# Kernel tuning notes

Hardware: AMD Instinct MI355X
Metric: run time of the kernel (lower is better)

## Reference

```python
import jax, jax.numpy as jnp
import numpy as np

D_MODEL = 1024
N_HEADS = 16
FF_DIM = 4096
EPS = 1e-05


def setup_inputs() -> dict:
    key = jax.random.key(0)
    ks = jax.random.split(key, 8)
    B, T, E, F = 4, 2048, D_MODEL, FF_DIM
    s = 0.02
    return {
        "encoder_input": jax.random.normal(ks[0], (B, T, E), jnp.float32),
        "source_padding_masks": jax.random.randint(ks[1], (B, T), 0, 2, jnp.int32),
        "Wq": jax.random.normal(ks[2], (E, E), jnp.float32) * s,
        "Wk": jax.random.normal(ks[3], (E, E), jnp.float32) * s,
        "Wv": jax.random.normal(ks[4], (E, E), jnp.float32) * s,
        "Wo": jax.random.normal(ks[5], (E, E), jnp.float32) * s,
        "w1": jax.random.normal(ks[6], (F, E), jnp.float32) * s,
        "b1": jnp.zeros((F,), jnp.float32),
        "w2": jax.random.normal(ks[7], (E, F), jnp.float32) * s,
        "b2": jnp.zeros((E,), jnp.float32),
        "ln_g": jnp.ones((E,), jnp.float32),
        "ln_b": jnp.zeros((E,), jnp.float32),
    }


def _layer_norm(x, g, b):
    # Faithful to the custom LayerNorm: unbiased std (ddof=1), eps added to sd.
    mean = jnp.mean(x, axis=-1, keepdims=True)
    sd = jnp.std(x, axis=-1, keepdims=True, ddof=1)
    return (x - mean) / (sd + EPS) * g + b


def reference(encoder_input, source_padding_masks, Wq, Wk, Wv, Wo, w1, b1, w2, b2, ln_g, ln_b):
    x = encoder_input
    B, T, E = x.shape
    H, hd = N_HEADS, E // N_HEADS

    q = (x @ Wq.T).reshape(B, T, H, hd).transpose(0, 2, 1, 3)  # [B,H,T,hd]
    k = (x @ Wk.T).reshape(B, T, H, hd).transpose(0, 2, 1, 3)
    v = (x @ Wv.T).reshape(B, T, H, hd).transpose(0, 2, 1, 3)

    scores = jnp.einsum("bhqd,bhkd->bhqk", q, k) / jnp.sqrt(jnp.float32(hd))
    key_mask = source_padding_masks[:, None, None, :]  # [B,1,1,T]
    scores = jnp.where(key_mask == 0, -jnp.inf, scores)
    attn = jax.nn.softmax(scores, axis=-1)
    attn = attn * source_padding_masks[:, None, :, None].astype(attn.dtype)  # query mask post-softmax

    ctx = jnp.einsum("bhqk,bhkd->bhqd", attn, v)
    ctx = ctx.transpose(0, 2, 1, 3).reshape(B, T, E)
    att_out = ctx @ Wo.T

    # residual block 1 (dropout is identity in eval)
    h = _layer_norm(att_out + x, ln_g, ln_b)

    ff = jax.nn.relu(h @ w1.T + b1) @ w2.T + b2
    # residual block 2 (same shared LayerNorm params)
    out = _layer_norm(ff + h, ln_g, ln_b)
    return out
```

## Files before the change

kernel.cpp:

```cpp
#include <hip/hip_runtime.h>
#include <hip/hip_bf16.h>


typedef __attribute__((ext_vector_type(8))) short  short8;
typedef __attribute__((ext_vector_type(4))) float  f32x4;
typedef __attribute__((ext_vector_type(4))) int    i32x4;
typedef __attribute__((ext_vector_type(4))) unsigned short u16x4;

__device__ inline float b2f(unsigned short u) {
    unsigned int x = ((unsigned int)u) << 16;
    return __builtin_bit_cast(float, x);
}
__device__ inline unsigned short f2b(float f) {
    return __builtin_bit_cast(unsigned short, __float2bfloat16(f));
}

__device__ inline void llds16(const unsigned short* g, unsigned short* l) {
    __builtin_amdgcn_global_load_lds(
        (const __attribute__((address_space(1))) unsigned int*)g,
        (__attribute__((address_space(3))) unsigned int*)l, 16, 0, 0);
}

__device__ inline int swz(int row, int col8) {
    return (row << 6) + (((col8 ^ (row >> 1)) & 7) << 3);
}

__global__ __launch_bounds__(256)
void cast_f32_bf16(const float* __restrict__ in, unsigned short* __restrict__ out,
                   int n4)
{
    int i = blockIdx.x * 256 + threadIdx.x;
    if (i >= n4) return;
    f32x4 v = *(const f32x4*)(in + (size_t)i * 4);
    u16x4 o;
    for (int j = 0; j < 4; ++j) o[j] = f2b(v[j]);
    *(u16x4*)(out + (size_t)i * 4) = o;
}

__global__ __launch_bounds__(256)
void mask_bf16(const int* __restrict__ m, unsigned short* __restrict__ mb, int n)
{
    int i = blockIdx.x * 256 + threadIdx.x;
    if (i < n) mb[i] = m[i] ? (unsigned short)0x3F80 : (unsigned short)0;
}

template <int BIAS, int RELU, int QKV>
__global__ __launch_bounds__(512, 2)
void gemm256(const unsigned short* __restrict__ A,
             const unsigned short* __restrict__ W,
             const float* __restrict__ bias,
             const int* __restrict__ mask,
             unsigned short* __restrict__ C0,
             unsigned short* __restrict__ C1,
             unsigned short* __restrict__ C2,
             int M, int N, int K)
{
    __shared__ __attribute__((aligned(16))) unsigned short a_s[2][256 * 64];
    __shared__ __attribute__((aligned(16))) unsigned short b_s[2][256 * 64];

    const int tid  = threadIdx.x;
    const int lane = tid & 63;
    const int w    = tid >> 6;
    const int ln   = lane & 15;
    const int quad = lane >> 4;
    const int wm   = w >> 2, wn = w & 3;
    const int bm   = blockIdx.y, bn = blockIdx.x;

    f32x4 acc[8][4] = {};

    auto stage = [&](int buf, int kt) {
#pragma unroll
        for (int i = 0; i < 4; ++i) {
            int e   = i * 512 + tid;
            int row = e >> 3;
            int c8  = (e & 7) ^ ((e >> 4) & 7);
            llds16(A + (size_t)(bm * 256 + row) * K + kt * 64 + c8 * 8,
                   &a_s[buf][e * 8]);
            llds16(W + (size_t)(bn * 256 + row) * K + kt * 64 + c8 * 8,
                   &b_s[buf][e * 8]);
        }
    };

    const int nkt = K >> 6;
    stage(0, 0);
    for (int kt = 0; kt < nkt; ++kt) {
        const int cur = kt & 1;
        asm volatile("s_waitcnt vmcnt(0)" ::: "memory");
        __builtin_amdgcn_s_barrier();
        if (kt + 1 < nkt) stage(cur ^ 1, kt + 1);
#pragma unroll
        for (int ks = 0; ks < 2; ++ks) {
            short8 af[8], bf_[4];
#pragma unroll
            for (int mt = 0; mt < 8; ++mt)
                af[mt] = *(const short8*)&a_s[cur][swz(wm * 128 + mt * 16 + ln, ks * 4 + quad)];
#pragma unroll
            for (int nt = 0; nt < 4; ++nt)
                bf_[nt] = *(const short8*)&b_s[cur][swz(wn * 64 + nt * 16 + ln, ks * 4 + quad)];
            __builtin_amdgcn_s_setprio(1);
#pragma unroll
            for (int mt = 0; mt < 8; ++mt)
#pragma unroll
                for (int nt = 0; nt < 4; ++nt)
                    acc[mt][nt] = __builtin_amdgcn_mfma_f32_16x16x32_bf16(
                        af[mt], bf_[nt], acc[mt][nt], 0, 0, 0);
            __builtin_amdgcn_s_setprio(0);
        }
    }

    const int crow0 = bm * 256 + wm * 128;
    const int ccol0 = bn * 256 + wn * 64;
    if (QKV) {
        const int seg  = bn >> 2;
        const int lc0  = ccol0 & 1023;
        if (seg < 2) {
            unsigned short* C = seg == 0 ? C0 : C1;
#pragma unroll
            for (int nt = 0; nt < 4; ++nt) {
                int col = lc0 + nt * 16 + ln;
#pragma unroll
                for (int mt = 0; mt < 8; ++mt) {
                    int row0 = crow0 + mt * 16 + quad * 4;
#pragma unroll
                    for (int r = 0; r < 4; ++r)
                        C[(size_t)(row0 + r) * 1024 + col] = f2b(acc[mt][nt][r]);
                }
            }
        } else {
            const int T2 = 2048, H2 = 16;
#pragma unroll
            for (int mt = 0; mt < 8; ++mt) {
                int row0 = crow0 + mt * 16 + quad * 4;
                int bb = row0 >> 11, t0 = row0 & 2047;
                i32x4 mi = *(const i32x4*)&mask[bb * 2048 + t0];
#pragma unroll
                for (int nt = 0; nt < 4; ++nt) {
                    int col = lc0 + nt * 16 + ln;
                    int hh2 = col >> 6, d = col & 63;
                    u16x4 o;
#pragma unroll
                    for (int r = 0; r < 4; ++r)
                        o[r] = mi[r] ? f2b(acc[mt][nt][r]) : (unsigned short)0;
                    *(u16x4*)(C2 + ((size_t)((bb * H2 + hh2) * 64 + d)) * T2 + t0) = o;
                }
            }
        }
    } else {
#pragma unroll
        for (int nt = 0; nt < 4; ++nt) {
            int col = ccol0 + nt * 16 + ln;
            float bv = 0.f;
            if (BIAS) bv = bias[col];
#pragma unroll
            for (int mt = 0; mt < 8; ++mt) {
                int row0 = crow0 + mt * 16 + quad * 4;
#pragma unroll
                for (int r = 0; r < 4; ++r) {
                    float v = acc[mt][nt][r] + bv;
                    if (RELU) v = v > 0.f ? v : 0.f;
                    C0[(size_t)(row0 + r) * N + col] = f2b(v);
                }
            }
        }
    }
}

__global__ __launch_bounds__(512, 2)
void flash_attn3(const unsigned short* __restrict__ Q,
                 const unsigned short* __restrict__ K,
                 const unsigned short* __restrict__ Vt,
                 const unsigned short* __restrict__ mb,
                 const int* __restrict__ mask,
                 unsigned short* __restrict__ O,
                 int T, int H, int E)
{
    __shared__ __attribute__((aligned(16))) unsigned short k_s[2][64 * 64];
    __shared__ __attribute__((aligned(16))) unsigned short v_s[2][64 * 64];
    __shared__ __attribute__((aligned(16))) unsigned short p_s[128 * 64];

    const int ord = blockIdx.x;
    const int wg  = (ord & 7) * 128 + (ord >> 3);
    const int qt  = wg & 15;
    const int h   = (wg >> 4) & 15;
    const int b   = wg >> 8;

    const int tid  = threadIdx.x;
    const int w    = tid >> 6;
    const int lane = tid & 63;
    const int ln   = lane & 15;
    const int quad = lane >> 4;
    const int q0   = qt * 128;
    const unsigned short* vt_b = Vt + (size_t)(b * H + h) * 64 * T;

    {
        int e = tid;
        int row = e >> 3;
        int c8  = (e & 7) ^ ((e >> 4) & 7);
        llds16(K + (size_t)(b * T + row) * E + h * 64 + c8 * 8, &k_s[0][e * 8]);
        llds16(vt_b + (size_t)row * T + c8 * 8, &v_s[0][e * 8]);
    }
    for (int i = 0; i < 2; ++i) {
        int e = i * 512 + tid;
        int row = e >> 3;
        int c8  = (e & 7) ^ ((e >> 4) & 7);
        llds16(Q + (size_t)(b * T + q0 + row) * E + h * 64 + c8 * 8, &p_s[e * 8]);
    }
    __syncthreads();
    short8 aq[2];
    aq[0] = *(const short8*)&p_s[w * 1024 + swz(ln, quad)];
    aq[1] = *(const short8*)&p_s[w * 1024 + swz(ln, 4 + quad)];

    f32x4 Oa[4] = {};
    f32x4 lacc = {};
    const float SCL = 0.125f * 1.44269504f;

    const int nkb = T >> 6;
    for (int kb = 0; kb < nkb; ++kb) {
        const int cur = kb & 1;
        if (kb + 1 < nkb) {
            int e = tid;
            int row = e >> 3;
            int c8  = (e & 7) ^ ((e >> 4) & 7);
            llds16(K + (size_t)(b * T + (kb + 1) * 64 + row) * E + h * 64 + c8 * 8,
                   &k_s[cur ^ 1][e * 8]);
            llds16(vt_b + (size_t)row * T + (kb + 1) * 64 + c8 * 8,
                   &v_s[cur ^ 1][e * 8]);
        }
        short8 mf0 = *(const short8*)&mb[b * T + kb * 64 + quad * 8];
        short8 mf1 = *(const short8*)&mb[b * T + kb * 64 + 32 + quad * 8];

        f32x4 S[4] = {};
        for (int ks = 0; ks < 2; ++ks)
            for (int nt = 0; nt < 4; ++nt) {
                short8 bf_ = *(const short8*)&k_s[cur][swz(nt * 16 + ln, ks * 4 + quad)];
                S[nt] = __builtin_amdgcn_mfma_f32_16x16x32_bf16(aq[ks], bf_, S[nt], 0, 0, 0);
            }
        for (int nt = 0; nt < 4; ++nt)
            for (int r = 0; r < 4; ++r) {
                float p = exp2f(S[nt][r] * SCL);
                p_s[w * 1024 + swz(quad * 4 + r, 2 * nt + (ln >> 3)) + (ln & 7)] = f2b(p);
            }
        short8 ap0 = *(const short8*)&p_s[w * 1024 + swz(ln, quad)];
        short8 ap1 = *(const short8*)&p_s[w * 1024 + swz(ln, 4 + quad)];
        lacc = __builtin_amdgcn_mfma_f32_16x16x32_bf16(ap0, mf0, lacc, 0, 0, 0);
        lacc = __builtin_amdgcn_mfma_f32_16x16x32_bf16(ap1, mf1, lacc, 0, 0, 0);
        for (int nt = 0; nt < 4; ++nt) {
            short8 bv0 = *(const short8*)&v_s[cur][swz(nt * 16 + ln, quad)];
            Oa[nt] = __builtin_amdgcn_mfma_f32_16x16x32_bf16(ap0, bv0, Oa[nt], 0, 0, 0);
            short8 bv1 = *(const short8*)&v_s[cur][swz(nt * 16 + ln, 4 + quad)];
            Oa[nt] = __builtin_amdgcn_mfma_f32_16x16x32_bf16(ap1, bv1, Oa[nt], 0, 0, 0);
        }
        __syncthreads();
    }

    for (int r = 0; r < 4; ++r) {
        int qrow = q0 + w * 16 + quad * 4 + r;
        float inv = mask[b * T + qrow] ? 1.f / lacc[r] : 0.f;
        for (int nt = 0; nt < 4; ++nt)
            O[(size_t)(b * T + qrow) * E + h * 64 + nt * 16 + ln] = f2b(Oa[nt][r] * inv);
    }
}

template <int R_F32, int O_F32>
__global__ __launch_bounds__(256, 4)
void ln_residual(const unsigned short* __restrict__ A,
                 const void* __restrict__ R,
                 const float* __restrict__ G,
                 const float* __restrict__ Bt,
                 void* __restrict__ Y, int E)
{
    const int row = blockIdx.x;
    const int tid = threadIdx.x;
    size_t base = (size_t)row * E + tid * 4;
    u16x4 a4 = *(const u16x4*)(A + base);
    float rv[4];
    if (R_F32) {
        f32x4 r4 = *(const f32x4*)((const float*)R + base);
        for (int j = 0; j < 4; ++j) rv[j] = r4[j];
    } else {
        u16x4 r4 = *(const u16x4*)((const unsigned short*)R + base);
        for (int j = 0; j < 4; ++j) rv[j] = b2f(r4[j]);
    }
    float v[4]; float s = 0.f, sq = 0.f;
    for (int j = 0; j < 4; ++j) {
        v[j] = b2f(a4[j]) + rv[j];
        s += v[j]; sq += v[j] * v[j];
    }
    for (int o = 32; o; o >>= 1) {
        s  += __shfl_xor(s, o, 64);
        sq += __shfl_xor(sq, o, 64);
    }
    __shared__ float red[8];
    int w = tid >> 6, lane = tid & 63;
    if (lane == 0) { red[w] = s; red[4 + w] = sq; }
    __syncthreads();
    s  = red[0] + red[1] + red[2] + red[3];
    sq = red[4] + red[5] + red[6] + red[7];
    float mean = s / E;
    float var  = (sq - s * mean) / (E - 1);
    var = fmaxf(var, 0.f);
    float inv = 1.f / (sqrtf(var) + 1e-5f);
    f32x4 g4 = *(const f32x4*)(G + tid * 4);
    f32x4 b4 = *(const f32x4*)(Bt + tid * 4);
    if (O_F32) {
        f32x4 o4;
        for (int j = 0; j < 4; ++j)
            o4[j] = (v[j] - mean) * inv * g4[j] + b4[j];
        *(f32x4*)((float*)Y + base) = o4;
    } else {
        u16x4 o4;
        for (int j = 0; j < 4; ++j)
            o4[j] = f2b((v[j] - mean) * inv * g4[j] + b4[j]);
        *(u16x4*)((unsigned short*)Y + base) = o4;
    }
}

extern "C" void kernel_launch(void* const* d_in, const int* in_sizes, int n_in,
                              void* d_out, int out_size, void* d_ws, size_t ws_size,
                              hipStream_t stream)
{
    const int B = 4, T = 2048, E = 1024, F = 4096, H = 16;
    const int M = B * T;

    const float* x  = (const float*)d_in[0];
    const int* mask = (const int*)d_in[1];
    const float* Wq = (const float*)d_in[2];
    const float* Wk = (const float*)d_in[3];
    const float* Wv = (const float*)d_in[4];
    const float* Wo = (const float*)d_in[5];
    const float* w1 = (const float*)d_in[6];
    const float* b1 = (const float*)d_in[7];
    const float* w2 = (const float*)d_in[8];
    const float* b2 = (const float*)d_in[9];
    const float* lg = (const float*)d_in[10];
    const float* lb = (const float*)d_in[11];
    float* out = (float*)d_out;

    char* ws = (char*)d_ws;
    const size_t MB = 1024 * 1024;
    unsigned short* xb  = (unsigned short*)(ws);
    unsigned short* q   = (unsigned short*)(ws + 16 * MB);
    unsigned short* kk  = (unsigned short*)(ws + 32 * MB);
    unsigned short* vt  = (unsigned short*)(ws + 48 * MB);
    unsigned short* ctx = (unsigned short*)(ws + 64 * MB);
    unsigned short* hh  = (unsigned short*)(ws + 80 * MB);
    unsigned short* mbf = hh;
    unsigned short* ff1 = (unsigned short*)(ws);
    unsigned short* ff2 = ctx;
    unsigned short* att = q;
    unsigned short* Wqb = (unsigned short*)(ws + 96 * MB);
    unsigned short* Wkb = (unsigned short*)(ws + 98 * MB);
    unsigned short* Wvb = (unsigned short*)(ws + 100 * MB);
    unsigned short* Wob = (unsigned short*)(ws + 102 * MB);
    unsigned short* w1b = (unsigned short*)(ws + 104 * MB);
    unsigned short* w2b = (unsigned short*)(ws + 112 * MB);

    dim3 blk(256);
    cast_f32_bf16<<<dim3(M * E / 4 / 256), blk, 0, stream>>>(x,  xb,  M * E / 4);
    cast_f32_bf16<<<dim3(E * E / 4 / 256), blk, 0, stream>>>(Wq, Wqb, E * E / 4);
    cast_f32_bf16<<<dim3(E * E / 4 / 256), blk, 0, stream>>>(Wk, Wkb, E * E / 4);
    cast_f32_bf16<<<dim3(E * E / 4 / 256), blk, 0, stream>>>(Wv, Wvb, E * E / 4);
    cast_f32_bf16<<<dim3(E * E / 4 / 256), blk, 0, stream>>>(Wo, Wob, E * E / 4);
    cast_f32_bf16<<<dim3(F * E / 4 / 256), blk, 0, stream>>>(w1, w1b, F * E / 4);
    cast_f32_bf16<<<dim3(F * E / 4 / 256), blk, 0, stream>>>(w2, w2b, F * E / 4);
    mask_bf16<<<dim3(M / 256), blk, 0, stream>>>(mask, mbf, M);

    dim3 g512(512);
    gemm256<0, 0, 1><<<dim3(3072 / 256, M / 256), g512, 0, stream>>>(
        xb, Wqb, nullptr, mask, q, kk, vt, M, 3072, E);
    flash_attn3<<<dim3((T / 128) * H * B), g512, 0, stream>>>(q, kk, vt, mbf, mask, ctx, T, H, E);
    gemm256<0, 0, 0><<<dim3(E / 256, M / 256), g512, 0, stream>>>(
        ctx, Wob, nullptr, nullptr, att, nullptr, nullptr, M, E, E);
    ln_residual<1, 0><<<dim3(M), blk, 0, stream>>>(att, x, lg, lb, hh, E);
    gemm256<1, 1, 0><<<dim3(F / 256, M / 256), g512, 0, stream>>>(
        hh, w1b, b1, nullptr, ff1, nullptr, nullptr, M, F, E);
    gemm256<1, 0, 0><<<dim3(E / 256, M / 256), g512, 0, stream>>>(
        ff1, w2b, b2, nullptr, ff2, nullptr, nullptr, M, E, F);
    ln_residual<0, 1><<<dim3(M), blk, 0, stream>>>(ff2, hh, lg, lb, out, E);
}
```

Baseline: 614.3 us.

## Shrink GEMM tiles to 128x128 with deeper prefetch and merge cast launches

The GEMM tile drops from 256x256 with 512 threads to 128x128 with 256 threads. The K-loop now issues loads two tiles ahead and uses a partial vmcnt wait instead of draining all loads each iteration. The seven separate f32-to-bf16 cast launches become one launch that maps block ranges to tensors. The smaller tiles mean more blocks, which fills the CUs better (for example the M=8192, N=1024 GEMMs go from 128 to 512 blocks), at the cost of lower operand reuse per block and an extra barrier each iteration.

```diff
diff --git a/kernel.cpp b/kernel.cpp
--- a/kernel.cpp
+++ b/kernel.cpp
@@ -25,16 +25,23 @@
     return (row << 6) + (((col8 ^ (row >> 1)) & 7) << 3);
 }
 
+struct CastArgs {
+    const float* src[7];
+    unsigned short* dst[7];
+    int blkcum[8];
+};
+
 __global__ __launch_bounds__(256)
-void cast_f32_bf16(const float* __restrict__ in, unsigned short* __restrict__ out,
-                   int n4)
-{
-    int i = blockIdx.x * 256 + threadIdx.x;
-    if (i >= n4) return;
-    f32x4 v = *(const f32x4*)(in + (size_t)i * 4);
+void cast_all(CastArgs a)
+{
+    int blk = blockIdx.x;
+    int s = 0;
+    while (blk >= a.blkcum[s + 1]) ++s;
+    int i = (blk - a.blkcum[s]) * 256 + threadIdx.x;
+    f32x4 v = *(const f32x4*)(a.src[s] + (size_t)i * 4);
     u16x4 o;
     for (int j = 0; j < 4; ++j) o[j] = f2b(v[j]);
-    *(u16x4*)(out + (size_t)i * 4) = o;
+    *(u16x4*)(a.dst[s] + (size_t)i * 4) = o;
 }
 
 __global__ __launch_bounds__(256)
@@ -45,8 +52,8 @@
 }
 
 template <int BIAS, int RELU, int QKV>
-__global__ __launch_bounds__(512, 2)
-void gemm256(const unsigned short* __restrict__ A,
+__global__ __launch_bounds__(256, 2)
+void gemm_db(const unsigned short* __restrict__ A,
              const unsigned short* __restrict__ W,
              const float* __restrict__ bias,
              const int* __restrict__ mask,
@@ -55,72 +62,73 @@
              unsigned short* __restrict__ C2,
              int M, int N, int K)
 {
-    __shared__ __attribute__((aligned(16))) unsigned short a_s[2][256 * 64];
-    __shared__ __attribute__((aligned(16))) unsigned short b_s[2][256 * 64];
+    __shared__ __attribute__((aligned(16))) unsigned short a_s[2][128 * 64];
+    __shared__ __attribute__((aligned(16))) unsigned short b_s[2][128 * 64];
 
     const int tid  = threadIdx.x;
     const int lane = tid & 63;
     const int w    = tid >> 6;
     const int ln   = lane & 15;
     const int quad = lane >> 4;
-    const int wm   = w >> 2, wn = w & 3;
+    const int wm   = w >> 1, wn = w & 1;
     const int bm   = blockIdx.y, bn = blockIdx.x;
 
-    f32x4 acc[8][4] = {};
+    f32x4 acc[4][4] = {};
+
+    const unsigned short* Abase = A + (size_t)(bm * 128) * K;
+    const unsigned short* Wbase = W + (size_t)(bn * 128) * K;
 
     auto stage = [&](int buf, int kt) {
 #pragma unroll
         for (int i = 0; i < 4; ++i) {
-            int e   = i * 512 + tid;
+            int e   = i * 256 + tid;
             int row = e >> 3;
             int c8  = (e & 7) ^ ((e >> 4) & 7);
-            llds16(A + (size_t)(bm * 256 + row) * K + kt * 64 + c8 * 8,
-                   &a_s[buf][e * 8]);
-            llds16(W + (size_t)(bn * 256 + row) * K + kt * 64 + c8 * 8,
-                   &b_s[buf][e * 8]);
+            llds16(Abase + (size_t)row * K + kt * 64 + c8 * 8, &a_s[buf][e * 8]);
+            llds16(Wbase + (size_t)row * K + kt * 64 + c8 * 8, &b_s[buf][e * 8]);
         }
     };
 
     const int nkt = K >> 6;
     stage(0, 0);
+    stage(1, 1);
+    int cur = 0;
     for (int kt = 0; kt < nkt; ++kt) {
-        const int cur = kt & 1;
-        asm volatile("s_waitcnt vmcnt(0)" ::: "memory");
-        __builtin_amdgcn_s_barrier();
-        if (kt + 1 < nkt) stage(cur ^ 1, kt + 1);
+        if (kt + 1 < nkt) asm volatile("s_waitcnt vmcnt(8)" ::: "memory");
+        else              asm volatile("s_waitcnt vmcnt(0)" ::: "memory");
+        asm volatile("s_barrier" ::: "memory");
 #pragma unroll
         for (int ks = 0; ks < 2; ++ks) {
-            short8 af[8], bf_[4];
-#pragma unroll
-            for (int mt = 0; mt < 8; ++mt)
-                af[mt] = *(const short8*)&a_s[cur][swz(wm * 128 + mt * 16 + ln, ks * 4 + quad)];
+            short8 af[4], bf_[4];
+#pragma unroll
+            for (int mt = 0; mt < 4; ++mt)
+                af[mt] = *(const short8*)&a_s[cur][swz(wm * 64 + mt * 16 + ln, ks * 4 + quad)];
 #pragma unroll
             for (int nt = 0; nt < 4; ++nt)
                 bf_[nt] = *(const short8*)&b_s[cur][swz(wn * 64 + nt * 16 + ln, ks * 4 + quad)];
-            __builtin_amdgcn_s_setprio(1);
-#pragma unroll
-            for (int mt = 0; mt < 8; ++mt)
+#pragma unroll
+            for (int mt = 0; mt < 4; ++mt)
 #pragma unroll
                 for (int nt = 0; nt < 4; ++nt)
                     acc[mt][nt] = __builtin_amdgcn_mfma_f32_16x16x32_bf16(
                         af[mt], bf_[nt], acc[mt][nt], 0, 0, 0);
-            __builtin_amdgcn_s_setprio(0);
-        }
-    }
-
-    const int crow0 = bm * 256 + wm * 128;
-    const int ccol0 = bn * 256 + wn * 64;
+        }
+        asm volatile("s_barrier" ::: "memory");
+        if (kt + 2 < nkt) stage(cur, kt + 2);
+        cur ^= 1;
+    }
+
     if (QKV) {
-        const int seg  = bn >> 2;
-        const int lc0  = ccol0 & 1023;
+        const int seg = bn >> 3;
+        const int lbn = bn & 7;
         if (seg < 2) {
             unsigned short* C = seg == 0 ? C0 : C1;
 #pragma unroll
             for (int nt = 0; nt < 4; ++nt) {
-                int col = lc0 + nt * 16 + ln;
-#pragma unroll
-                for (int mt = 0; mt < 8; ++mt) {
-                    int row0 = crow0 + mt * 16 + quad * 4;
+                int col = lbn * 128 + wn * 64 + nt * 16 + ln;
+#pragma unroll
+                for (int mt = 0; mt < 4; ++mt) {
+                    int row0 = bm * 128 + wm * 64 + mt * 16 + quad * 4;
 #pragma unroll
                     for (int r = 0; r < 4; ++r)
                         C[(size_t)(row0 + r) * 1024 + col] = f2b(acc[mt][nt][r]);
@@ -129,13 +137,13 @@
         } else {
             const int T2 = 2048, H2 = 16;
 #pragma unroll
-            for (int mt = 0; mt < 8; ++mt) {
-                int row0 = crow0 + mt * 16 + quad * 4;
+            for (int mt = 0; mt < 4; ++mt) {
+                int row0 = bm * 128 + wm * 64 + mt * 16 + quad * 4;
                 int bb = row0 >> 11, t0 = row0 & 2047;
                 i32x4 mi = *(const i32x4*)&mask[bb * 2048 + t0];
 #pragma unroll
                 for (int nt = 0; nt < 4; ++nt) {
-                    int col = lc0 + nt * 16 + ln;
+                    int col = lbn * 128 + wn * 64 + nt * 16 + ln;
                     int hh2 = col >> 6, d = col & 63;
                     u16x4 o;
 #pragma unroll
@@ -148,12 +156,12 @@
     } else {
 #pragma unroll
         for (int nt = 0; nt < 4; ++nt) {
-            int col = ccol0 + nt * 16 + ln;
+            int col = bn * 128 + wn * 64 + nt * 16 + ln;
             float bv = 0.f;
             if (BIAS) bv = bias[col];
 #pragma unroll
-            for (int mt = 0; mt < 8; ++mt) {
-                int row0 = crow0 + mt * 16 + quad * 4;
+            for (int mt = 0; mt < 4; ++mt) {
+                int row0 = bm * 128 + wm * 64 + mt * 16 + quad * 4;
 #pragma unroll
                 for (int r = 0; r < 4; ++r) {
                     float v = acc[mt][nt][r] + bv;
@@ -356,25 +364,32 @@
     unsigned short* w2b = (unsigned short*)(ws + 112 * MB);
 
     dim3 blk(256);
-    cast_f32_bf16<<<dim3(M * E / 4 / 256), blk, 0, stream>>>(x,  xb,  M * E / 4);
-    cast_f32_bf16<<<dim3(E * E / 4 / 256), blk, 0, stream>>>(Wq, Wqb, E * E / 4);
-    cast_f32_bf16<<<dim3(E * E / 4 / 256), blk, 0, stream>>>(Wk, Wkb, E * E / 4);
-    cast_f32_bf16<<<dim3(E * E / 4 / 256), blk, 0, stream>>>(Wv, Wvb, E * E / 4);
-    cast_f32_bf16<<<dim3(E * E / 4 / 256), blk, 0, stream>>>(Wo, Wob, E * E / 4);
-    cast_f32_bf16<<<dim3(F * E / 4 / 256), blk, 0, stream>>>(w1, w1b, F * E / 4);
-    cast_f32_bf16<<<dim3(F * E / 4 / 256), blk, 0, stream>>>(w2, w2b, F * E / 4);
+    dim3 g512(512);
+
+    CastArgs ca;
+    ca.src[0] = x;  ca.dst[0] = xb;
+    ca.src[1] = Wq; ca.dst[1] = Wqb;
+    ca.src[2] = Wk; ca.dst[2] = Wkb;
+    ca.src[3] = Wv; ca.dst[3] = Wvb;
+    ca.src[4] = Wo; ca.dst[4] = Wob;
+    ca.src[5] = w1; ca.dst[5] = w1b;
+    ca.src[6] = w2; ca.dst[6] = w2b;
+    int blks[7] = { M * E / 1024, E * E / 1024, E * E / 1024, E * E / 1024,
+                    E * E / 1024, F * E / 1024, F * E / 1024 };
+    ca.blkcum[0] = 0;
+    for (int i = 0; i < 7; ++i) ca.blkcum[i + 1] = ca.blkcum[i] + blks[i];
+    cast_all<<<dim3(ca.blkcum[7]), blk, 0, stream>>>(ca);
     mask_bf16<<<dim3(M / 256), blk, 0, stream>>>(mask, mbf, M);
 
-    dim3 g512(512);
-    gemm256<0, 0, 1><<<dim3(3072 / 256, M / 256), g512, 0, stream>>>(
+    gemm_db<0, 0, 1><<<dim3(3072 / 128, M / 128), blk, 0, stream>>>(
         xb, Wqb, nullptr, mask, q, kk, vt, M, 3072, E);
     flash_attn3<<<dim3((T / 128) * H * B), g512, 0, stream>>>(q, kk, vt, mbf, mask, ctx, T, H, E);
-    gemm256<0, 0, 0><<<dim3(E / 256, M / 256), g512, 0, stream>>>(
+    gemm_db<0, 0, 0><<<dim3(E / 128, M / 128), blk, 0, stream>>>(
         ctx, Wob, nullptr, nullptr, att, nullptr, nullptr, M, E, E);
     ln_residual<1, 0><<<dim3(M), blk, 0, stream>>>(att, x, lg, lb, hh, E);
-    gemm256<1, 1, 0><<<dim3(F / 256, M / 256), g512, 0, stream>>>(
+    gemm_db<1, 1, 0><<<dim3(F / 128, M / 128), blk, 0, stream>>>(
         hh, w1b, b1, nullptr, ff1, nullptr, nullptr, M, F, E);
-    gemm256<1, 0, 0><<<dim3(E / 256, M / 256), g512, 0, stream>>>(
+    gemm_db<1, 0, 0><<<dim3(E / 128, M / 128), blk, 0, stream>>>(
         ff1, w2b, b2, nullptr, ff2, nullptr, nullptr, M, E, F);
     ln_residual<0, 1><<<dim3(M), blk, 0, stream>>>(ff2, hh, lg, lb, out, E);
 }
```

After: 520.8 us. 1.18x faster.
